# Kernel tuning notes

Hardware: AMD Instinct MI355X
Metric: run time of the kernel (lower is better)

## Reference

```python
import jax, jax.numpy as jnp
import numpy as np

H, D, E, S_E, P_E, N, B = 16, 48, 768, 384, 128, 768, 1

def _ln(x, g=None, b=None, eps=1e-5):
    mu = jnp.mean(x, axis=-1, keepdims=True)
    var = jnp.var(x, axis=-1, keepdims=True)
    y = (x - mu) * jax.lax.rsqrt(var + eps)
    if g is not None:
        y = y * g
    if b is not None:
        y = y + b
    return y

def setup_inputs() -> dict:
    key = jax.random.key(0)
    ks = jax.random.split(key, 16)
    sc_e = 1.0 / np.sqrt(E)
    sc_s = 1.0 / np.sqrt(S_E)
    sc_p = 1.0 / np.sqrt(P_E)
    return {
        "a": jax.random.normal(ks[0], (B, N, E), jnp.float32),
        "s": jax.random.normal(ks[1], (B, N, S_E), jnp.float32),
        "pair_rep": jax.random.normal(ks[2], (B, N, N, P_E), jnp.float32),
        "beta": jax.random.normal(ks[3], (B, N, N), jnp.float32),
        # AdaLN: sigmoid-gated scale and shift from s
        "w_ada_gamma": jax.random.normal(ks[4], (S_E, E), jnp.float32) * sc_s,
        "w_ada_beta": jax.random.normal(ks[5], (S_E, E), jnp.float32) * sc_s,
        # q/k/v projections, stored as [E, H, D]
        "wq": jax.random.normal(ks[6], (E, H, D), jnp.float32) * sc_e,
        "bq": jnp.zeros((H, D), jnp.float32),
        "wk": jax.random.normal(ks[7], (E, H, D), jnp.float32) * sc_e,
        "wv": jax.random.normal(ks[8], (E, H, D), jnp.float32) * sc_e,
        # pair bias: LayerNorm(P_E) + Linear(P_E -> H, no bias)
        "ln_pair_g": jnp.ones((P_E,), jnp.float32),
        "ln_pair_b": jnp.zeros((P_E,), jnp.float32),
        "w_pair": jax.random.normal(ks[9], (P_E, H), jnp.float32) * sc_p,
        # gate projection [E, H, D], no bias, sigmoid
        "w_gate": jax.random.normal(ks[10], (E, H, D), jnp.float32) * sc_e,
        # output projections
        "w_proj_a": jax.random.normal(ks[11], (E, E), jnp.float32) * sc_e,
        "w_out": jax.random.normal(ks[12], (S_E, E), jnp.float32) * sc_s,
        "b_out": jnp.full((E,), -2.0, jnp.float32),
    }

def reference(a, s, pair_rep, beta, w_ada_gamma, w_ada_beta, wq, bq, wk, wv,
              ln_pair_g, ln_pair_b, w_pair, w_gate, w_proj_a, w_out, b_out):
    # AdaLN: normalize a (no affine); gamma/beta conditioned on normalized s
    a_n = _ln(a)
    s_n = _ln(s)
    gamma = jax.nn.sigmoid(s_n @ w_ada_gamma)
    a_mod = gamma * a_n + s_n @ w_ada_beta            # [B,N,E]

    q = jnp.einsum('bne,ehd->bnhd', a_mod, wq) + bq   # [B,N,H,D]
    k = jnp.einsum('bne,ehd->bnhd', a_mod, wk)
    v = jnp.einsum('bne,ehd->bnhd', a_mod, wv)
    g = jax.nn.sigmoid(jnp.einsum('bne,ehd->bnhd', a_mod, w_gate))

    # per-head pair bias: LN(pair) @ w_pair + beta -> [B,H,N,N]
    b = jnp.einsum('bnmp,ph->bhnm', _ln(pair_rep, ln_pair_g, ln_pair_b), w_pair)
    b = b + beta[:, None, :, :]

    scale = 1.0 / np.sqrt(D)
    logits = jnp.einsum('bnhd,bmhd->bhnm', q, k) * scale + b
    weights = jax.nn.softmax(logits, axis=-1)         # [B,H,N,N]

    attn = jnp.einsum('bhnm,bmhd->bhnd', weights, v)
    attn = attn * jnp.moveaxis(g, -2, -3)             # gate per head
    attn = jnp.moveaxis(attn, -3, -2).reshape(a.shape[0], a.shape[1], H * D)
    out = attn @ w_proj_a                             # [B,N,E]
    out = jax.nn.sigmoid(s @ w_out + b_out) * out
    return out
```

## Files before the change

### kernel.cpp

```cpp
#include <hip/hip_runtime.h>
#include <hip/hip_bf16.h>

typedef __attribute__((ext_vector_type(8))) short short8;
typedef __attribute__((ext_vector_type(8))) unsigned short u16x8;
typedef __attribute__((ext_vector_type(4))) unsigned short u16x4;
typedef __attribute__((ext_vector_type(4))) float f32x4;
typedef __attribute__((ext_vector_type(4))) unsigned u32x4;

#define NTOK 768
#define ED   768
#define SD   384
#define PD   128
#define NH   16
#define DH   48

__device__ __forceinline__ unsigned short f2bf(float x) {
  unsigned u = __builtin_bit_cast(unsigned, x);
  u += 0x7FFFu + ((u >> 16) & 1u);
  return (unsigned short)(u >> 16);
}
__device__ __forceinline__ float bf2f(unsigned short b) {
  unsigned u = ((unsigned)b) << 16;
  return __builtin_bit_cast(float, u);
}
__device__ __forceinline__ float sigm(float x) { return 1.0f / (1.0f + __expf(-x)); }

__device__ __forceinline__ unsigned cvtpk(float a, float b) {
  unsigned r;
  asm("v_cvt_pk_bf16_f32 %0, %1, %2" : "=v"(r) : "v"(a), "v"(b));
  return r;
}
__device__ __forceinline__ float lo2f(unsigned p) {
  return __builtin_bit_cast(float, p << 16);
}
__device__ __forceinline__ float hi2f(unsigned p) {
  return __builtin_bit_cast(float, p & 0xFFFF0000u);
}

__device__ __forceinline__ void gl2lds(const unsigned short* g, unsigned short* l) {
  __builtin_amdgcn_global_load_lds(
      (const __attribute__((address_space(1))) unsigned int*)g,
      (__attribute__((address_space(3))) unsigned int*)l, 16, 0, 0);
}

constexpr size_t SZ_SN   = (size_t)NTOK * SD * 2;
constexpr size_t OFF_SNH = 0;
constexpr size_t OFF_SNL = OFF_SNH + SZ_SN;
constexpr size_t OFF_SRH = OFF_SNL + SZ_SN;
constexpr size_t OFF_SRL = OFF_SRH + SZ_SN;
constexpr size_t OFF_GAM = OFF_SRL + SZ_SN;
constexpr size_t OFF_BET = OFF_GAM + 2359296;
constexpr size_t OFF_OG  = OFF_BET + 2359296;
constexpr size_t OFF_AMH = OFF_OG  + 2359296;
constexpr size_t OFF_AML = OFF_AMH + 1179648;
constexpr size_t OFF_QB  = OFF_AML + 1179648;
constexpr size_t OFF_KB  = OFF_QB  + 1179648;
constexpr size_t OFF_VT  = OFF_KB  + 1179648;
constexpr size_t OFF_GBUF= OFF_VT  + 1179648;
constexpr size_t OFF_AGH = OFF_GBUF+ 2359296;
constexpr size_t OFF_AGL = OFF_AGH + 1179648;
constexpr size_t OFF_WSMH= OFF_AGL + 1179648;
constexpr size_t OFF_WSML= OFF_WSMH+ 1769472;
constexpr size_t OFF_WQH = OFF_WSML+ 1769472;
constexpr size_t OFF_WQL = OFF_WQH + 4718592;
constexpr size_t OFF_WPH = OFF_WQL + 4718592;
constexpr size_t OFF_WPL = OFF_WPH + 1179648;
constexpr size_t OFF_GWH = OFF_WPL + 1179648;
constexpr size_t OFF_GWL = OFF_GWH + 4096;
constexpr size_t OFF_SGW = OFF_GWL + 4096;
constexpr size_t OFF_QKL = OFF_SGW + 4096;
constexpr size_t OFF_PB  = OFF_QKL + 37748736;
constexpr size_t WS_NEED = OFF_PB  + 18874368;

__global__ __launch_bounds__(256) void k_wcvt(
    const float* __restrict__ wag, const float* __restrict__ wab, const float* __restrict__ wo,
    const float* __restrict__ wq, const float* __restrict__ wk, const float* __restrict__ wv,
    const float* __restrict__ wg, const float* __restrict__ wp,
    const float* __restrict__ lng, const float* __restrict__ lnb,
    const float* __restrict__ wpair, const float* __restrict__ s,
    unsigned short* __restrict__ wsmh, unsigned short* __restrict__ wsml,
    unsigned short* __restrict__ wqh, unsigned short* __restrict__ wql,
    unsigned short* __restrict__ wph, unsigned short* __restrict__ wpl,
    unsigned short* __restrict__ gwh, unsigned short* __restrict__ gwl,
    float* __restrict__ sgw, float* __restrict__ bw,
    unsigned short* __restrict__ snh, unsigned short* __restrict__ snl,
    unsigned short* __restrict__ srh, unsigned short* __restrict__ srl) {
  const int tid = threadIdx.x;
  if (blockIdx.z == 8) {
    const int gid = blockIdx.y * 24 + blockIdx.x;
    if (gid == 192) {
      if (tid < 128) {
        float g = lng[tid];
        for (int hh = 0; hh < 16; ++hh) {
          float gwv = g * wpair[tid * 16 + hh];
          unsigned short hb = f2bf(gwv);
          gwh[tid * 16 + hh] = hb;
          gwl[tid * 16 + hh] = f2bf(gwv - bf2f(hb));
        }
      }
      if (tid < 16) {
        float sv = 0.f, bb = 0.f;
        for (int p = 0; p < 128; ++p) {
          float w = wpair[p * 16 + tid];
          sv += lng[p] * w;
          bb += lnb[p] * w;
        }
        sgw[tid] = sv;
        bw[tid]  = bb;
      }
      return;
    }
    if (gid > 192) return;
    const int n = gid * 4 + (tid >> 6);
    const int lane = tid & 63;
    const float* row = s + (size_t)n * SD;
    float v[6], sum = 0.f, sq = 0.f;
#pragma unroll
    for (int i = 0; i < 6; ++i) { v[i] = row[lane + 64 * i]; sum += v[i]; sq += v[i] * v[i]; }
#pragma unroll
    for (int off = 1; off < 64; off <<= 1) { sum += __shfl_xor(sum, off); sq += __shfl_xor(sq, off); }
    float mu = sum * (1.f / SD);
    float var = sq * (1.f / SD) - mu * mu;
    float rs = rsqrtf(var + 1e-5f);
#pragma unroll
    for (int i = 0; i < 6; ++i) {
      size_t idx = (size_t)n * SD + lane + 64 * i;
      float x = v[i];
      unsigned short xh = f2bf(x);
      srh[idx] = xh; srl[idx] = f2bf(x - bf2f(xh));
      float y = (x - mu) * rs;
      unsigned short yh = f2bf(y);
      snh[idx] = yh; snl[idx] = f2bf(y - bf2f(yh));
    }
    return;
  }
  const int id = blockIdx.z;
  const float* src; int Ksrc; unsigned short *dh, *dl; int n0; int Kd;
  switch (id) {
    case 0: src = wag; Ksrc = 384; dh = wsmh; dl = wsml; n0 = 0;    Kd = 384; break;
    case 1: src = wab; Ksrc = 384; dh = wsmh; dl = wsml; n0 = 768;  Kd = 384; break;
    case 2: src = wo;  Ksrc = 384; dh = wsmh; dl = wsml; n0 = 1536; Kd = 384; break;
    case 3: src = wq;  Ksrc = 768; dh = wqh;  dl = wql;  n0 = 0;    Kd = 768; break;
    case 4: src = wk;  Ksrc = 768; dh = wqh;  dl = wql;  n0 = 768;  Kd = 768; break;
    case 5: src = wv;  Ksrc = 768; dh = wqh;  dl = wql;  n0 = 1536; Kd = 768; break;
    case 6: src = wg;  Ksrc = 768; dh = wqh;  dl = wql;  n0 = 2304; Kd = 768; break;
    default: src = wp; Ksrc = 768; dh = wph;  dl = wpl;  n0 = 0;    Kd = 768; break;
  }
  const int kt = blockIdx.x, ntile = blockIdx.y;
  if (kt * 32 >= Ksrc) return;
  __shared__ float t[32][33];
  const int r = tid >> 3, c4 = (tid & 7) * 4;
  float4 v = *(const float4*)(src + (size_t)(kt * 32 + r) * 768 + ntile * 32 + c4);
  t[r][c4 + 0] = v.x; t[r][c4 + 1] = v.y; t[r][c4 + 2] = v.z; t[r][c4 + 3] = v.w;
  __syncthreads();
  u16x4 hv, lv;
#pragma unroll
  for (int j = 0; j < 4; ++j) {
    float x = t[c4 + j][r];
    unsigned short hb = f2bf(x);
    hv[j] = hb;
    lv[j] = f2bf(x - bf2f(hb));
  }
  size_t drow = (size_t)(n0 + ntile * 32 + r) * Kd + kt * 32 + c4;
  *(u16x4*)(dh + drow) = hv;
  *(u16x4*)(dl + drow) = lv;
}

__device__ __forceinline__ void mfma_core(
    const unsigned short* __restrict__ Ah, const unsigned short* __restrict__ Al,
    const unsigned short* __restrict__ Bh, const unsigned short* __restrict__ Bl,
    int K, int mBase, int nBase, f32x4 acc[4][4]) {
  __shared__ unsigned short lds[2][4][8192];
  const int tid = threadIdx.x;
  const int w = tid >> 6, lane = tid & 63;
  const int l15 = lane & 15, kg = lane >> 4;
  const int wr = w >> 1, wc = w & 1;

  size_t offA[4], offB[4];
  int ldsw[4];
#pragma unroll
  for (int i = 0; i < 4; ++i) {
    int chunk = w * 256 + i * 64 + lane;
    int row = chunk >> 3;
    int slot = (chunk & 7) ^ (row & 7);
    offA[i] = (size_t)(mBase + row) * K + slot * 8;
    offB[i] = (size_t)(nBase + row) * K + slot * 8;
    ldsw[i] = w * 2048 + i * 512;
  }
  auto stage = [&](int b, int k0) {
#pragma unroll
    for (int i = 0; i < 4; ++i) {
      gl2lds(Ah + offA[i] + k0, &lds[b][0][ldsw[i]]);
      gl2lds(Al + offA[i] + k0, &lds[b][1][ldsw[i]]);
      gl2lds(Bh + offB[i] + k0, &lds[b][2][ldsw[i]]);
      gl2lds(Bl + offB[i] + k0, &lds[b][3][ldsw[i]]);
    }
  };

  stage(0, 0);
  int buf = 0;
  for (int k0 = 64; k0 <= K; k0 += 64) {
    __syncthreads();
    if (k0 < K) stage(buf ^ 1, k0);
#pragma unroll
    for (int kk = 0; kk < 2; ++kk) {
      short8 ah[4], al[4], bh4[4], bl4[4];
#pragma unroll
      for (int mi = 0; mi < 4; ++mi) {
        int row = wr * 64 + mi * 16 + l15;
        int kb = kk * 64 + kg * 16;
        int idx = row * 64 + ((kb ^ ((row & 7) << 4)) >> 1);
        ah[mi] = *(const short8*)&lds[buf][0][idx];
        al[mi] = *(const short8*)&lds[buf][1][idx];
      }
#pragma unroll
      for (int ni = 0; ni < 4; ++ni) {
        int row = wc * 64 + ni * 16 + l15;
        int kb = kk * 64 + kg * 16;
        int idx = row * 64 + ((kb ^ ((row & 7) << 4)) >> 1);
        bh4[ni] = *(const short8*)&lds[buf][2][idx];
        bl4[ni] = *(const short8*)&lds[buf][3][idx];
      }
#pragma unroll
      for (int mi = 0; mi < 4; ++mi)
#pragma unroll
        for (int ni = 0; ni < 4; ++ni) {
          acc[mi][ni] = __builtin_amdgcn_mfma_f32_16x16x32_bf16(ah[mi], bh4[ni], acc[mi][ni], 0, 0, 0);
          acc[mi][ni] = __builtin_amdgcn_mfma_f32_16x16x32_bf16(al[mi], bh4[ni], acc[mi][ni], 0, 0, 0);
          acc[mi][ni] = __builtin_amdgcn_mfma_f32_16x16x32_bf16(ah[mi], bl4[ni], acc[mi][ni], 0, 0, 0);
        }
    }
    buf ^= 1;
  }
}

__global__ __launch_bounds__(256) void k_gemm_small(
    const unsigned short* __restrict__ snh, const unsigned short* __restrict__ snl,
    const unsigned short* __restrict__ srh, const unsigned short* __restrict__ srl,
    const unsigned short* __restrict__ wsmh, const unsigned short* __restrict__ wsml,
    const float* __restrict__ bo,
    float* __restrict__ gaml, float* __restrict__ betl, float* __restrict__ og) {
  const int nt = blockIdx.x, mt = blockIdx.y;
  const unsigned short* Ah = (nt < 12) ? snh : srh;
  const unsigned short* Al = (nt < 12) ? snl : srl;
  f32x4 acc[4][4];
#pragma unroll
  for (int i = 0; i < 4; ++i)
#pragma unroll
    for (int j = 0; j < 4; ++j) acc[i][j] = (f32x4){0.f, 0.f, 0.f, 0.f};
  mfma_core(Ah, Al, wsmh, wsml, SD, mt * 128, nt * 128, acc);
  const int tid = threadIdx.x;
  const int w = tid >> 6, lane = tid & 63;
  const int l15 = lane & 15, kg = lane >> 4;
  const int wr = w >> 1, wc = w & 1;
#pragma unroll
  for (int mi = 0; mi < 4; ++mi)
#pragma unroll
    for (int ni = 0; ni < 4; ++ni) {
      int col = nt * 128 + wc * 64 + ni * 16 + l15;
#pragma unroll
      for (int r = 0; r < 4; ++r) {
        int row = mt * 128 + wr * 64 + mi * 16 + kg * 4 + r;
        float v = acc[mi][ni][r];
        if (col < 768) gaml[(size_t)row * ED + col] = v;
        else if (col < 1536) betl[(size_t)row * ED + col - 768] = v;
        else og[(size_t)row * ED + col - 1536] = sigm(v + bo[col - 1536]);
      }
    }
}

__global__ __launch_bounds__(256) void k_gemm_qkvg(
    const unsigned short* __restrict__ amh, const unsigned short* __restrict__ aml,
    const unsigned short* __restrict__ wqh, const unsigned short* __restrict__ wql,
    const float* __restrict__ bq,
    unsigned short* __restrict__ qb, unsigned short* __restrict__ kb,
    unsigned short* __restrict__ vT, float* __restrict__ gbuf) {
  const int nt = blockIdx.x, mt = blockIdx.y;
  f32x4 acc[4][4];
#pragma unroll
  for (int i = 0; i < 4; ++i)
#pragma unroll
    for (int j = 0; j < 4; ++j) acc[i][j] = (f32x4){0.f, 0.f, 0.f, 0.f};
  mfma_core(amh, aml, wqh, wql, ED, mt * 128, nt * 128, acc);
  const int tid = threadIdx.x;
  const int w = tid >> 6, lane = tid & 63;
  const int l15 = lane & 15, kg = lane >> 4;
  const int wr = w >> 1, wc = w & 1;
  const int sel = nt / 6;
#pragma unroll
  for (int mi = 0; mi < 4; ++mi)
#pragma unroll
    for (int ni = 0; ni < 4; ++ni) {
      int col = nt * 128 + wc * 64 + ni * 16 + l15;
      int c = col - sel * 768;
#pragma unroll
      for (int r = 0; r < 4; ++r) {
        int row = mt * 128 + wr * 64 + mi * 16 + kg * 4 + r;
        float v = acc[mi][ni][r];
        size_t idx = (size_t)row * ED + c;
        if (sel == 0) qb[idx] = f2bf(v + bq[c]);
        else if (sel == 1) kb[idx] = f2bf(v);
        else if (sel == 2) vT[(size_t)c * NTOK + row] = f2bf(v);
        else gbuf[idx] = sigm(v);
      }
    }
}

__global__ __launch_bounds__(256) void k_gemm_proj(
    const unsigned short* __restrict__ agh, const unsigned short* __restrict__ agl,
    const unsigned short* __restrict__ wph, const unsigned short* __restrict__ wpl,
    const float* __restrict__ og, float* __restrict__ out) {
  const int nt = blockIdx.x, mt = blockIdx.y;
  f32x4 acc[4][4];
#pragma unroll
  for (int i = 0; i < 4; ++i)
#pragma unroll
    for (int j = 0; j < 4; ++j) acc[i][j] = (f32x4){0.f, 0.f, 0.f, 0.f};
  mfma_core(agh, agl, wph, wpl, ED, mt * 128, nt * 128, acc);
  const int tid = threadIdx.x;
  const int w = tid >> 6, lane = tid & 63;
  const int l15 = lane & 15, kg = lane >> 4;
  const int wr = w >> 1, wc = w & 1;
#pragma unroll
  for (int mi = 0; mi < 4; ++mi)
#pragma unroll
    for (int ni = 0; ni < 4; ++ni) {
      int col = nt * 128 + wc * 64 + ni * 16 + l15;
#pragma unroll
      for (int r = 0; r < 4; ++r) {
        int row = mt * 128 + wr * 64 + mi * 16 + kg * 4 + r;
        size_t idx = (size_t)row * ED + col;
        out[idx] = acc[mi][ni][r] * og[idx];
      }
    }
}

__global__ __launch_bounds__(256) void k_amod(const float* __restrict__ a,
                                              const float* __restrict__ gamma_lin,
                                              const float* __restrict__ beta_lin,
                                              unsigned short* __restrict__ amh,
                                              unsigned short* __restrict__ aml) {
  __shared__ float red[8];
  const int n = blockIdx.x, tid = threadIdx.x;
  const int lane = tid & 63, wid = tid >> 6;
  const float* row = a + (size_t)n * ED;
  float v[3], sum = 0.f, sq = 0.f;
#pragma unroll
  for (int i = 0; i < 3; ++i) { v[i] = row[tid + 256 * i]; sum += v[i]; sq += v[i] * v[i]; }
#pragma unroll
  for (int off = 1; off < 64; off <<= 1) { sum += __shfl_xor(sum, off); sq += __shfl_xor(sq, off); }
  if (lane == 0) { red[wid] = sum; red[4 + wid] = sq; }
  __syncthreads();
  float S = red[0] + red[1] + red[2] + red[3];
  float Q = red[4] + red[5] + red[6] + red[7];
  float mu = S * (1.f / ED);
  float var = Q * (1.f / ED) - mu * mu;
  float rs = rsqrtf(var + 1e-5f);
#pragma unroll
  for (int i = 0; i < 3; ++i) {
    int e = tid + 256 * i;
    float an = (v[i] - mu) * rs;
    size_t idx = (size_t)n * ED + e;
    float val = sigm(gamma_lin[idx]) * an + beta_lin[idx];
    unsigned short h = f2bf(val);
    amh[idx] = h;
    aml[idx] = f2bf(val - bf2f(h));
  }
}

__global__ __launch_bounds__(256) void k_qkw(const unsigned short* __restrict__ qb,
                                             const unsigned short* __restrict__ kb,
                                             const float* __restrict__ beta,
                                             float* __restrict__ qkl) {
  const int mt = blockIdx.x, ntile = blockIdx.y, h = blockIdx.z;
  __shared__ unsigned short qs[64 * 72];
  __shared__ unsigned short ksm[64 * 72];
  const int tid = threadIdx.x;
  const int n0 = ntile * 64, m0 = mt * 64;
  const u16x8 z = {0, 0, 0, 0, 0, 0, 0, 0};
#pragma unroll
  for (int it = 0; it < 2; ++it) {
    int idx = tid + it * 256;
    int row = idx >> 3, c = idx & 7;
    u16x8 vq = z, vk = z;
    if (c < 6) {
      vq = *(const u16x8*)(qb + (size_t)(n0 + row) * ED + h * DH + c * 8);
      vk = *(const u16x8*)(kb + (size_t)(m0 + row) * ED + h * DH + c * 8);
    }
    *(u16x8*)(qs + row * 72 + c * 8) = vq;
    *(u16x8*)(ksm + row * 72 + c * 8) = vk;
  }
  __syncthreads();
  const int wv = tid >> 6, lane = tid & 63;
  const int l15 = lane & 15, kg = lane >> 4;
  f32x4 acc[4];
#pragma unroll
  for (int ct = 0; ct < 4; ++ct) acc[ct] = (f32x4){0.f, 0.f, 0.f, 0.f};
#pragma unroll
  for (int ks2 = 0; ks2 < 2; ++ks2) {
    short8 av = *(const short8*)(qs + (wv * 16 + l15) * 72 + ks2 * 32 + kg * 8);
#pragma unroll
    for (int ct = 0; ct < 4; ++ct) {
      short8 bv = *(const short8*)(ksm + (ct * 16 + l15) * 72 + ks2 * 32 + kg * 8);
      acc[ct] = __builtin_amdgcn_mfma_f32_16x16x32_bf16(av, bv, acc[ct], 0, 0, 0);
    }
  }
  const float scale = 0.14433756729740643f;
#pragma unroll
  for (int ct = 0; ct < 4; ++ct)
#pragma unroll
    for (int r = 0; r < 4; ++r) {
      int nn = n0 + wv * 16 + kg * 4 + r;
      int mm = m0 + ct * 16 + l15;
      qkl[((size_t)nn * NH + h) * NTOK + mm] =
          fmaf(acc[ct][r], scale, beta[(size_t)nn * NTOK + mm]);
    }
}

__global__ __launch_bounds__(256, 3) void k_pairsm(const float* __restrict__ pair_rep,
                                                   const float* __restrict__ qkl,
                                                   const unsigned short* __restrict__ gw_hi,
                                                   const unsigned short* __restrict__ gw_lo,
                                                   const float* __restrict__ sgw, const float* __restrict__ bw,
                                                   unsigned short* __restrict__ pb) {
  __shared__ float lg[16 * 776];
  const int n = blockIdx.x;
  const int tid = threadIdx.x;
  const int wv = tid >> 6, lane = tid & 63;
  const int l15 = lane & 15, kg = lane >> 4;

#define LOADCH(X, CH) do {                                                        \
    const float* xp_ = pair_rep + ((size_t)n * NTOK + (CH) * 16 + l15) * PD + kg * 8; \
    _Pragma("unroll")                                                             \
    for (int q_ = 0; q_ < 4; ++q_) {                                              \
      X[q_ * 2]     = *(const float4*)(xp_ + q_ * 32);                            \
      X[q_ * 2 + 1] = *(const float4*)(xp_ + q_ * 32 + 4);                        \
    }                                                                             \
  } while (0)

  float4 Xa[8], Xb[8];
  LOADCH(Xa, wv);

  {
    const float4* src = (const float4*)(qkl + (size_t)n * (NH * NTOK));
    for (int i = tid; i < 3072; i += 256) {
      float4 v = src[i];
      int h = i / 192;
      int m = (i - h * 192) * 4;
      *(float4*)&lg[h * 776 + m] = v;
    }
  }

  short8 bh[4], bl[4];
#pragma unroll
  for (int ks = 0; ks < 4; ++ks)
#pragma unroll
    for (int j = 0; j < 8; ++j) {
      int p = ks * 32 + kg * 8 + j;
      bh[ks][j] = (short)gw_hi[p * 16 + l15];
      bl[ks][j] = (short)gw_lo[p * 16 + l15];
    }
  float sgv[4], bwv[4];
#pragma unroll
  for (int r = 0; r < 4; ++r) { sgv[r] = sgw[kg * 4 + r]; bwv[r] = bw[kg * 4 + r]; }

  __syncthreads();

#define PROC(X, CH) do {                                                          \
    float sum_ = 0.f, sq_ = 0.f;                                                  \
    _Pragma("unroll")                                                             \
    for (int q_ = 0; q_ < 8; ++q_) {                                              \
      sum_ += X[q_].x + X[q_].y + X[q_].z + X[q_].w;                              \
      sq_ = fmaf(X[q_].x, X[q_].x, sq_); sq_ = fmaf(X[q_].y, X[q_].y, sq_);       \
      sq_ = fmaf(X[q_].z, X[q_].z, sq_); sq_ = fmaf(X[q_].w, X[q_].w, sq_);       \
    }                                                                             \
    sum_ += __shfl_xor(sum_, 16); sum_ += __shfl_xor(sum_, 32);                   \
    sq_  += __shfl_xor(sq_, 16);  sq_  += __shfl_xor(sq_, 32);                    \
    float mu_ = sum_ * (1.f / 128.f);                                             \
    float rstd_ = rsqrtf(sq_ * (1.f / 128.f) - mu_ * mu_ + 1e-5f);                \
    f32x4 acc_ = {0.f, 0.f, 0.f, 0.f};                                            \
    _Pragma("unroll")                                                             \
    for (int ks_ = 0; ks_ < 4; ++ks_) {                                           \
      float4 u0_ = X[ks_ * 2], u1_ = X[ks_ * 2 + 1];                              \
      unsigned p0_ = cvtpk(u0_.x, u0_.y), p1_ = cvtpk(u0_.z, u0_.w);              \
      unsigned p2_ = cvtpk(u1_.x, u1_.y), p3_ = cvtpk(u1_.z, u1_.w);              \
      float l0_ = u0_.x - lo2f(p0_), l1_ = u0_.y - hi2f(p0_);                     \
      float l2_ = u0_.z - lo2f(p1_), l3_ = u0_.w - hi2f(p1_);                     \
      float l4_ = u1_.x - lo2f(p2_), l5_ = u1_.y - hi2f(p2_);                     \
      float l6_ = u1_.z - lo2f(p3_), l7_ = u1_.w - hi2f(p3_);                     \
      unsigned q0_ = cvtpk(l0_, l1_), q1_ = cvtpk(l2_, l3_);                      \
      unsigned q2_ = cvtpk(l4_, l5_), q3_ = cvtpk(l6_, l7_);                      \
      u32x4 hp_ = {p0_, p1_, p2_, p3_}, lp_ = {q0_, q1_, q2_, q3_};               \
      short8 ah_ = __builtin_bit_cast(short8, hp_);                               \
      short8 al_ = __builtin_bit_cast(short8, lp_);                               \
      acc_ = __builtin_amdgcn_mfma_f32_16x16x32_bf16(bh[ks_], ah_, acc_, 0, 0, 0);\
      acc_ = __builtin_amdgcn_mfma_f32_16x16x32_bf16(bh[ks_], al_, acc_, 0, 0, 0);\
      acc_ = __builtin_amdgcn_mfma_f32_16x16x32_bf16(bl[ks_], ah_, acc_, 0, 0, 0);\
    }                                                                             \
    _Pragma("unroll")                                                             \
    for (int r_ = 0; r_ < 4; ++r_) {                                              \
      float val_ = rstd_ * (acc_[r_] - mu_ * sgv[r_]) + bwv[r_];                  \
      lg[(kg * 4 + r_) * 776 + (CH) * 16 + l15] += val_;                          \
    }                                                                             \
  } while (0)

  LOADCH(Xb, wv + 4);   PROC(Xa, wv);
  LOADCH(Xa, wv + 8);   PROC(Xb, wv + 4);
  LOADCH(Xb, wv + 12);  PROC(Xa, wv + 8);
  LOADCH(Xa, wv + 16);  PROC(Xb, wv + 12);
  LOADCH(Xb, wv + 20);  PROC(Xa, wv + 16);
  LOADCH(Xa, wv + 24);  PROC(Xb, wv + 20);
  LOADCH(Xb, wv + 28);  PROC(Xa, wv + 24);
  LOADCH(Xa, wv + 32);  PROC(Xb, wv + 28);
  LOADCH(Xb, wv + 36);  PROC(Xa, wv + 32);
  LOADCH(Xa, wv + 40);  PROC(Xb, wv + 36);
  LOADCH(Xb, wv + 44);  PROC(Xa, wv + 40);
                        PROC(Xb, wv + 44);
#undef LOADCH
#undef PROC
  __syncthreads();

#pragma unroll
  for (int hh = 0; hh < 4; ++hh) {
    int h = wv * 4 + hh;
    float x[12];
#pragma unroll
    for (int i = 0; i < 12; ++i) x[i] = lg[h * 776 + lane + 64 * i];
    float mx = x[0];
#pragma unroll
    for (int t = 1; t < 12; ++t) mx = fmaxf(mx, x[t]);
#pragma unroll
    for (int off = 1; off < 64; off <<= 1) mx = fmaxf(mx, __shfl_xor(mx, off));
    float e[12], sm = 0.f;
#pragma unroll
    for (int t = 0; t < 12; ++t) { e[t] = __expf(x[t] - mx); sm += e[t]; }
#pragma unroll
    for (int off = 1; off < 64; off <<= 1) sm += __shfl_xor(sm, off);
    float inv = 1.0f / sm;
    unsigned short* dst = pb + ((size_t)h * NTOK + n) * NTOK;
#pragma unroll
    for (int i = 0; i < 12; ++i) dst[lane + 64 * i] = f2bf(e[i] * inv);
  }
}

__global__ __launch_bounds__(256) void k_pv(const unsigned short* __restrict__ wb,
                                            const unsigned short* __restrict__ vT,
                                            const float* __restrict__ gbuf,
                                            unsigned short* __restrict__ agh,
                                            unsigned short* __restrict__ agl) {
  const int ntile = blockIdx.x, h = blockIdx.y;
  const int n0 = ntile * 64;
  __shared__ unsigned short wsm[64 * 40];
  __shared__ unsigned short vtm[48 * 40];
  const int tid = threadIdx.x;
  const int wv = tid >> 6, lane = tid & 63, l15 = lane & 15, kg = lane >> 4;
  f32x4 acc[3];
#pragma unroll
  for (int dt = 0; dt < 3; ++dt) acc[dt] = (f32x4){0.f, 0.f, 0.f, 0.f};
  for (int k0 = 0; k0 < NTOK; k0 += 32) {
    __syncthreads();
    {
      int row = tid >> 2, c = tid & 3;
      *(u16x8*)(wsm + row * 40 + c * 8) =
          *(const u16x8*)(wb + ((size_t)h * NTOK + (n0 + row)) * NTOK + k0 + c * 8);
    }
    if (tid < 192) {
      int d = tid >> 2, c = tid & 3;
      *(u16x8*)(vtm + d * 40 + c * 8) =
          *(const u16x8*)(vT + (size_t)(h * DH + d) * NTOK + k0 + c * 8);
    }
    __syncthreads();
    short8 av = *(const short8*)(wsm + (wv * 16 + l15) * 40 + kg * 8);
#pragma unroll
    for (int dt = 0; dt < 3; ++dt) {
      short8 bv = *(const short8*)(vtm + (dt * 16 + l15) * 40 + kg * 8);
      acc[dt] = __builtin_amdgcn_mfma_f32_16x16x32_bf16(av, bv, acc[dt], 0, 0, 0);
    }
  }
#pragma unroll
  for (int dt = 0; dt < 3; ++dt)
#pragma unroll
    for (int r = 0; r < 4; ++r) {
      int nn = n0 + wv * 16 + kg * 4 + r;
      int col = h * DH + dt * 16 + l15;
      size_t idx = (size_t)nn * ED + col;
      float val = acc[dt][r] * gbuf[idx];
      unsigned short hb = f2bf(val);
      agh[idx] = hb;
      agl[idx] = f2bf(val - bf2f(hb));
    }
}

extern "C" void kernel_launch(void* const* d_in, const int* in_sizes, int n_in,
                              void* d_out, int out_size, void* d_ws, size_t ws_size,
                              hipStream_t stream) {
  const float* a    = (const float*)d_in[0];
  const float* s    = (const float*)d_in[1];
  const float* pair = (const float*)d_in[2];
  const float* beta = (const float*)d_in[3];
  const float* wag  = (const float*)d_in[4];
  const float* wab  = (const float*)d_in[5];
  const float* wq   = (const float*)d_in[6];
  const float* bq   = (const float*)d_in[7];
  const float* wk   = (const float*)d_in[8];
  const float* wvp  = (const float*)d_in[9];
  const float* lng  = (const float*)d_in[10];
  const float* lnb  = (const float*)d_in[11];
  const float* wpair= (const float*)d_in[12];
  const float* wg   = (const float*)d_in[13];
  const float* wproj= (const float*)d_in[14];
  const float* wo   = (const float*)d_in[15];
  const float* bo   = (const float*)d_in[16];
  float* out = (float*)d_out;

  if (ws_size < WS_NEED) return;

  char* ws = (char*)d_ws;
  unsigned short* snh  = (unsigned short*)(ws + OFF_SNH);
  unsigned short* snl  = (unsigned short*)(ws + OFF_SNL);
  unsigned short* srh  = (unsigned short*)(ws + OFF_SRH);
  unsigned short* srl  = (unsigned short*)(ws + OFF_SRL);
  float*          gaml = (float*)(ws + OFF_GAM);
  float*          betl = (float*)(ws + OFF_BET);
  float*          og   = (float*)(ws + OFF_OG);
  unsigned short* amh  = (unsigned short*)(ws + OFF_AMH);
  unsigned short* aml  = (unsigned short*)(ws + OFF_AML);
  unsigned short* qb   = (unsigned short*)(ws + OFF_QB);
  unsigned short* kb   = (unsigned short*)(ws + OFF_KB);
  unsigned short* vT   = (unsigned short*)(ws + OFF_VT);
  float*          gbuf = (float*)(ws + OFF_GBUF);
  unsigned short* agh  = (unsigned short*)(ws + OFF_AGH);
  unsigned short* agl  = (unsigned short*)(ws + OFF_AGL);
  unsigned short* wsmh = (unsigned short*)(ws + OFF_WSMH);
  unsigned short* wsml = (unsigned short*)(ws + OFF_WSML);
  unsigned short* wqh  = (unsigned short*)(ws + OFF_WQH);
  unsigned short* wql  = (unsigned short*)(ws + OFF_WQL);
  unsigned short* wph  = (unsigned short*)(ws + OFF_WPH);
  unsigned short* wpl  = (unsigned short*)(ws + OFF_WPL);
  unsigned short* gwh  = (unsigned short*)(ws + OFF_GWH);
  unsigned short* gwl  = (unsigned short*)(ws + OFF_GWL);
  float*          sgw  = (float*)(ws + OFF_SGW);
  float*          bw   = sgw + 16;
  float*          qkl  = (float*)(ws + OFF_QKL);
  unsigned short* pb   = (unsigned short*)(ws + OFF_PB);

  hipLaunchKernelGGL(k_wcvt, dim3(24, 24, 9), dim3(256), 0, stream,
                     wag, wab, wo, wq, wk, wvp, wg, wproj, lng, lnb, wpair, s,
                     wsmh, wsml, wqh, wql, wph, wpl, gwh, gwl, sgw, bw,
                     snh, snl, srh, srl);
  hipLaunchKernelGGL(k_gemm_small, dim3(18, 6), dim3(256), 0, stream,
                     snh, snl, srh, srl, wsmh, wsml, bo, gaml, betl, og);
  hipLaunchKernelGGL(k_amod, dim3(768), dim3(256), 0, stream, a, gaml, betl, amh, aml);
  hipLaunchKernelGGL(k_gemm_qkvg, dim3(24, 6), dim3(256), 0, stream,
                     amh, aml, wqh, wql, bq, qb, kb, vT, gbuf);
  hipLaunchKernelGGL(k_qkw, dim3(12, 12, 16), dim3(256), 0, stream, qb, kb, beta, qkl);
  hipLaunchKernelGGL(k_pairsm, dim3(768), dim3(256), 0, stream,
                     pair, qkl, gwh, gwl, sgw, bw, pb);
  hipLaunchKernelGGL(k_pv, dim3(12, 16), dim3(256), 0, stream, pb, vT, gbuf, agh, agl);
  hipLaunchKernelGGL(k_gemm_proj, dim3(6, 6), dim3(256), 0, stream,
                     agh, agl, wph, wpl, og, out);
}
```

Baseline: 205.2 us.

## Fuse QK logits computation into pair-bias softmax kernel, drop qkl buffer

Removes the separate MFMA QK-logit kernel and its 37 MB fp32 intermediate. Each pair-softmax block now computes its row of q·k logits plus beta directly with scalar FMAs, reading bf16 K from global. The pair_rep prefetch is also reordered so two chunks are in flight before the logit computation. This trades a large global write/read for redundant scalar compute: every block rereads the full 1.2 MB K matrix, and the tensor-core path becomes per-thread FMA loops.

```diff
diff --git a/kernel.cpp b/kernel.cpp
--- a/kernel.cpp
+++ b/kernel.cpp
@@ -68,8 +68,7 @@
 constexpr size_t OFF_GWH = OFF_WPL + 1179648;
 constexpr size_t OFF_GWL = OFF_GWH + 4096;
 constexpr size_t OFF_SGW = OFF_GWL + 4096;
-constexpr size_t OFF_QKL = OFF_SGW + 4096;
-constexpr size_t OFF_PB  = OFF_QKL + 37748736;
+constexpr size_t OFF_PB  = OFF_SGW + 4096;
 constexpr size_t WS_NEED = OFF_PB  + 18874368;
 
 __global__ __launch_bounds__(256) void k_wcvt(
@@ -368,62 +367,16 @@
   }
 }
 
-__global__ __launch_bounds__(256) void k_qkw(const unsigned short* __restrict__ qb,
-                                             const unsigned short* __restrict__ kb,
-                                             const float* __restrict__ beta,
-                                             float* __restrict__ qkl) {
-  const int mt = blockIdx.x, ntile = blockIdx.y, h = blockIdx.z;
-  __shared__ unsigned short qs[64 * 72];
-  __shared__ unsigned short ksm[64 * 72];
-  const int tid = threadIdx.x;
-  const int n0 = ntile * 64, m0 = mt * 64;
-  const u16x8 z = {0, 0, 0, 0, 0, 0, 0, 0};
-#pragma unroll
-  for (int it = 0; it < 2; ++it) {
-    int idx = tid + it * 256;
-    int row = idx >> 3, c = idx & 7;
-    u16x8 vq = z, vk = z;
-    if (c < 6) {
-      vq = *(const u16x8*)(qb + (size_t)(n0 + row) * ED + h * DH + c * 8);
-      vk = *(const u16x8*)(kb + (size_t)(m0 + row) * ED + h * DH + c * 8);
-    }
-    *(u16x8*)(qs + row * 72 + c * 8) = vq;
-    *(u16x8*)(ksm + row * 72 + c * 8) = vk;
-  }
-  __syncthreads();
-  const int wv = tid >> 6, lane = tid & 63;
-  const int l15 = lane & 15, kg = lane >> 4;
-  f32x4 acc[4];
-#pragma unroll
-  for (int ct = 0; ct < 4; ++ct) acc[ct] = (f32x4){0.f, 0.f, 0.f, 0.f};
-#pragma unroll
-  for (int ks2 = 0; ks2 < 2; ++ks2) {
-    short8 av = *(const short8*)(qs + (wv * 16 + l15) * 72 + ks2 * 32 + kg * 8);
-#pragma unroll
-    for (int ct = 0; ct < 4; ++ct) {
-      short8 bv = *(const short8*)(ksm + (ct * 16 + l15) * 72 + ks2 * 32 + kg * 8);
-      acc[ct] = __builtin_amdgcn_mfma_f32_16x16x32_bf16(av, bv, acc[ct], 0, 0, 0);
-    }
-  }
-  const float scale = 0.14433756729740643f;
-#pragma unroll
-  for (int ct = 0; ct < 4; ++ct)
-#pragma unroll
-    for (int r = 0; r < 4; ++r) {
-      int nn = n0 + wv * 16 + kg * 4 + r;
-      int mm = m0 + ct * 16 + l15;
-      qkl[((size_t)nn * NH + h) * NTOK + mm] =
-          fmaf(acc[ct][r], scale, beta[(size_t)nn * NTOK + mm]);
-    }
-}
-
 __global__ __launch_bounds__(256, 3) void k_pairsm(const float* __restrict__ pair_rep,
-                                                   const float* __restrict__ qkl,
+                                                   const unsigned short* __restrict__ qb,
+                                                   const unsigned short* __restrict__ kb,
+                                                   const float* __restrict__ beta,
                                                    const unsigned short* __restrict__ gw_hi,
                                                    const unsigned short* __restrict__ gw_lo,
                                                    const float* __restrict__ sgw, const float* __restrict__ bw,
                                                    unsigned short* __restrict__ pb) {
   __shared__ float lg[16 * 776];
+  __shared__ float ql[768];
   const int n = blockIdx.x;
   const int tid = threadIdx.x;
   const int wv = tid >> 6, lane = tid & 63;
@@ -440,15 +393,12 @@
 
   float4 Xa[8], Xb[8];
   LOADCH(Xa, wv);
-
-  {
-    const float4* src = (const float4*)(qkl + (size_t)n * (NH * NTOK));
-    for (int i = tid; i < 3072; i += 256) {
-      float4 v = src[i];
-      int h = i / 192;
-      int m = (i - h * 192) * 4;
-      *(float4*)&lg[h * 776 + m] = v;
-    }
+  LOADCH(Xb, wv + 4);
+
+  if (tid < 96) {
+    u16x8 qv = *(const u16x8*)(qb + (size_t)n * ED + tid * 8);
+#pragma unroll
+    for (int i = 0; i < 8; ++i) ql[tid * 8 + i] = bf2f(qv[i]);
   }
 
   short8 bh[4], bl[4];
@@ -464,6 +414,38 @@
 #pragma unroll
   for (int r = 0; r < 4; ++r) { sgv[r] = sgw[kg * 4 + r]; bwv[r] = bw[kg * 4 + r]; }
 
+  __syncthreads();
+
+  {
+    const float scale = 0.14433756729740643f;
+    float bet0 = beta[(size_t)n * NTOK + tid];
+    float bet1 = beta[(size_t)n * NTOK + tid + 256];
+    float bet2 = beta[(size_t)n * NTOK + tid + 512];
+    const unsigned short* k0p = kb + (size_t)tid * ED;
+    const unsigned short* k1p = kb + (size_t)(tid + 256) * ED;
+    const unsigned short* k2p = kb + (size_t)(tid + 512) * ED;
+    for (int h = 0; h < 16; ++h) {
+      float a0 = 0.f, a1 = 0.f, a2 = 0.f;
+#pragma unroll
+      for (int d8 = 0; d8 < 6; ++d8) {
+        float4 q0 = *(const float4*)&ql[h * DH + d8 * 8];
+        float4 q1 = *(const float4*)&ql[h * DH + d8 * 8 + 4];
+        u16x8 k0 = *(const u16x8*)(k0p + h * DH + d8 * 8);
+        u16x8 k1 = *(const u16x8*)(k1p + h * DH + d8 * 8);
+        u16x8 k2 = *(const u16x8*)(k2p + h * DH + d8 * 8);
+        float qv[8] = {q0.x, q0.y, q0.z, q0.w, q1.x, q1.y, q1.z, q1.w};
+#pragma unroll
+        for (int i = 0; i < 8; ++i) {
+          a0 = fmaf(bf2f(k0[i]), qv[i], a0);
+          a1 = fmaf(bf2f(k1[i]), qv[i], a1);
+          a2 = fmaf(bf2f(k2[i]), qv[i], a2);
+        }
+      }
+      lg[h * 776 + tid      ] = fmaf(a0, scale, bet0);
+      lg[h * 776 + tid + 256] = fmaf(a1, scale, bet1);
+      lg[h * 776 + tid + 512] = fmaf(a2, scale, bet2);
+    }
+  }
   __syncthreads();
 
 #define PROC(X, CH) do {                                                          \
@@ -504,18 +486,18 @@
     }                                                                             \
   } while (0)
 
-  LOADCH(Xb, wv + 4);   PROC(Xa, wv);
-  LOADCH(Xa, wv + 8);   PROC(Xb, wv + 4);
-  LOADCH(Xb, wv + 12);  PROC(Xa, wv + 8);
-  LOADCH(Xa, wv + 16);  PROC(Xb, wv + 12);
-  LOADCH(Xb, wv + 20);  PROC(Xa, wv + 16);
-  LOADCH(Xa, wv + 24);  PROC(Xb, wv + 20);
-  LOADCH(Xb, wv + 28);  PROC(Xa, wv + 24);
-  LOADCH(Xa, wv + 32);  PROC(Xb, wv + 28);
-  LOADCH(Xb, wv + 36);  PROC(Xa, wv + 32);
-  LOADCH(Xa, wv + 40);  PROC(Xb, wv + 36);
-  LOADCH(Xb, wv + 44);  PROC(Xa, wv + 40);
-                        PROC(Xb, wv + 44);
+  PROC(Xa, wv +  0); LOADCH(Xa, wv +  8);
+  PROC(Xb, wv +  4); LOADCH(Xb, wv + 12);
+  PROC(Xa, wv +  8); LOADCH(Xa, wv + 16);
+  PROC(Xb, wv + 12); LOADCH(Xb, wv + 20);
+  PROC(Xa, wv + 16); LOADCH(Xa, wv + 24);
+  PROC(Xb, wv + 20); LOADCH(Xb, wv + 28);
+  PROC(Xa, wv + 24); LOADCH(Xa, wv + 32);
+  PROC(Xb, wv + 28); LOADCH(Xb, wv + 36);
+  PROC(Xa, wv + 32); LOADCH(Xa, wv + 40);
+  PROC(Xb, wv + 36); LOADCH(Xb, wv + 44);
+  PROC(Xa, wv + 40);
+  PROC(Xb, wv + 44);
 #undef LOADCH
 #undef PROC
   __syncthreads();
@@ -641,7 +623,6 @@
   unsigned short* gwl  = (unsigned short*)(ws + OFF_GWL);
   float*          sgw  = (float*)(ws + OFF_SGW);
   float*          bw   = sgw + 16;
-  float*          qkl  = (float*)(ws + OFF_QKL);
   unsigned short* pb   = (unsigned short*)(ws + OFF_PB);
 
   hipLaunchKernelGGL(k_wcvt, dim3(24, 24, 9), dim3(256), 0, stream,
@@ -653,9 +634,8 @@
   hipLaunchKernelGGL(k_amod, dim3(768), dim3(256), 0, stream, a, gaml, betl, amh, aml);
   hipLaunchKernelGGL(k_gemm_qkvg, dim3(24, 6), dim3(256), 0, stream,
                      amh, aml, wqh, wql, bq, qb, kb, vT, gbuf);
-  hipLaunchKernelGGL(k_qkw, dim3(12, 12, 16), dim3(256), 0, stream, qb, kb, beta, qkl);
   hipLaunchKernelGGL(k_pairsm, dim3(768), dim3(256), 0, stream,
-                     pair, qkl, gwh, gwl, sgw, bw, pb);
+                     pair, qb, kb, beta, gwh, gwl, sgw, bw, pb);
   hipLaunchKernelGGL(k_pv, dim3(12, 16), dim3(256), 0, stream, pb, vT, gbuf, agh, agl);
   hipLaunchKernelGGL(k_gemm_proj, dim3(6, 6), dim3(256), 0, stream,
                      agh, agl, wph, wpl, og, out);
```

New measurement: 384.3 us. +87.3%, slower.
